# Kernel optimization log

Measured on AMD Instinct MI355X. Metric: run time of the kernel, lower is better.

Reference implementation:

```python
import jax, jax.numpy as jnp
import numpy as np


def setup_inputs() -> dict:
    key = jax.random.key(0)
    k1, k2 = jax.random.split(key)
    batch, cw_dim = 4096, 1024
    dim_embedding, book_size = 8, 256
    dim_codes = cw_dim // dim_embedding  # 128
    x = jax.random.normal(k1, (batch, cw_dim), dtype=jnp.float32)
    codebook = jax.random.normal(k2, (dim_codes, book_size, dim_embedding), dtype=jnp.float32)
    return {"x": x, "codebook": codebook}


def reference(x, codebook):
    # Faithful JAX version of VQVAE.quantise:
    #   pairwise squared distance -> argmin -> gather embeddings -> one-hot scatter
    C, K, D = codebook.shape          # dim_codes, book_size, dim_embedding
    B = x.shape[0]
    xr = x.reshape(B, C, D)           # [B, C, D] (= view(batch*dim_codes, 1, D))
    x2 = jnp.sum(xr * xr, axis=-1)                       # [B, C]
    c2 = jnp.sum(codebook * codebook, axis=-1)           # [C, K]
    dist = x2[..., None] - 2.0 * jnp.einsum('bcd,ckd->bck', xr, codebook) + c2[None]
    idx = jnp.argmin(dist, axis=-1)                      # [B, C]
    # gather nearest codebook entry per code slot
    cw_embed = codebook[jnp.arange(C)[None, :], idx]     # [B, C, D]
    cw_embed = cw_embed.reshape(B, C * D)                # [B, cw_dim]
    # one-hot scatter of selected indices
    one_hot_idx = jax.nn.one_hot(idx, K, dtype=jnp.float32)  # [B, C, K]
    return cw_embed, one_hot_idx
```

## Files before the change

kernel.cpp:

```cpp
#include <hip/hip_runtime.h>


constexpr int B_  = 4096;
constexpr int C_  = 128;
constexpr int K_  = 256;
constexpr int D_  = 8;
constexpr int TPB = 256;

constexpr int   BPT   = 2;
constexpr int   BTILE = TPB * BPT;
constexpr float TAU2  = 1.0e-3f;

typedef float vf4 __attribute__((ext_vector_type(4)));

__global__ __launch_bounds__(TPB) void vq_fused(
    const float* __restrict__ x,
    const float* __restrict__ cb,
    float* __restrict__ out_embed,
    float* __restrict__ out_onehot)
{
    __shared__ float s_cbf[K_ * D_];
    __shared__ float s_c2f[K_];

    const int c    = blockIdx.x;
    const int bt   = blockIdx.y;
    const int tid  = threadIdx.x;
    const int lane = tid & 63;
    const int wave = tid >> 6;

    {
        const float4* gcb = (const float4*)(cb + (size_t)c * (K_ * D_));
        ((float4*)s_cbf)[tid]       = gcb[tid];
        ((float4*)s_cbf)[tid + TPB] = gcb[tid + TPB];
    }
    __syncthreads();
    {
        const float* v = s_cbf + tid * D_;
        float s = 0.f;
        #pragma unroll
        for (int d = 0; d < D_; ++d) s = fmaf(v[d], v[d], s);
        s_c2f[tid] = s;
    }
    __syncthreads();

    const float4* scb4 = (const float4*)s_cbf;
    const int bbase = bt * BTILE;

    float xf[BPT][D_];
    #pragma unroll
    for (int j = 0; j < BPT; ++j) {
        const int b = bbase + j * TPB + tid;
        const float4* xp = (const float4*)(x + (size_t)b * (C_ * D_) + c * D_);
        const float4 a = xp[0];
        const float4 h = xp[1];
        xf[j][0] = a.x; xf[j][1] = a.y; xf[j][2] = a.z; xf[j][3] = a.w;
        xf[j][4] = h.x; xf[j][5] = h.y; xf[j][6] = h.z; xf[j][7] = h.w;
    }

    float s1[BPT], s2[BPT];
    int   k1[BPT];
    #pragma unroll
    for (int j = 0; j < BPT; ++j) { s1[j] = 3.4e38f; s2[j] = 3.4e38f; k1[j] = 0; }

    #pragma unroll 2
    for (int k = 0; k < K_; ++k) {
        const float4 clo = scb4[k * 2];
        const float4 chi = scb4[k * 2 + 1];
        const float  c2k = s_c2f[k];
        #pragma unroll
        for (int j = 0; j < BPT; ++j) {
            float dot = xf[j][0] * clo.x;
            dot = fmaf(xf[j][1], clo.y, dot);
            dot = fmaf(xf[j][2], clo.z, dot);
            dot = fmaf(xf[j][3], clo.w, dot);
            dot = fmaf(xf[j][4], chi.x, dot);
            dot = fmaf(xf[j][5], chi.y, dot);
            dot = fmaf(xf[j][6], chi.z, dot);
            dot = fmaf(xf[j][7], chi.w, dot);
            const float score = fmaf(-2.f, dot, c2k);
            s2[j] = fminf(s2[j], fmaxf(score, s1[j]));
            const bool lt = score < s1[j];
            k1[j] = lt ? k : k1[j];
            s1[j] = lt ? score : s1[j];
        }
    }

    #pragma unroll
    for (int j = 0; j < BPT; ++j) {
        const bool amb = (s2[j] - s1[j]) <= TAU2;
        unsigned long long mask = __ballot(amb);
        while (mask) {
            const int src = (int)__ffsll((long long)mask) - 1;
            mask &= mask - 1;
            double xd[D_];
            #pragma unroll
            for (int d = 0; d < D_; ++d) xd[d] = (double)__shfl(xf[j][d], src);
            double best = 1.0e300;
            int    bk   = 0;
            #pragma unroll
            for (int t = 0; t < 4; ++t) {
                const int k = lane * 4 + t;
                const float* cv = s_cbf + k * D_;
                double cd[D_];
                #pragma unroll
                for (int d = 0; d < D_; ++d) cd[d] = (double)cv[d];
                double c2k = 0.0;
                #pragma unroll
                for (int d = 0; d < D_; ++d) c2k = fma(cd[d], cd[d], c2k);
                double dot = xd[0] * cd[0];
                #pragma unroll
                for (int d = 1; d < D_; ++d) dot = fma(xd[d], cd[d], dot);
                const double score = fma(-2.0, dot, c2k);
                if (score < best) { best = score; bk = k; }
            }
            #pragma unroll
            for (int off = 32; off >= 1; off >>= 1) {
                const double ob  = __shfl_down(best, off);
                const int    obk = __shfl_down(bk,   off);
                if (ob < best) { best = ob; bk = obk; }
            }
            const int win = __shfl(bk, 0);
            if (lane == src) k1[j] = win;
        }
    }

    #pragma unroll
    for (int j = 0; j < BPT; ++j) {
        const int    b    = bbase + j * TPB + tid;
        const size_t pair = (size_t)b * C_ + c;
        float4* dst = (float4*)(out_embed + pair * D_);
        dst[0] = ((const float4*)s_cbf)[k1[j] * 2];
        dst[1] = ((const float4*)s_cbf)[k1[j] * 2 + 1];

        const int bw = bbase + j * TPB + wave * 64;
        const int e0 = lane * 4;
        #pragma unroll 8
        for (int i = 0; i < 64; ++i) {
            const int k = __builtin_amdgcn_readlane(k1[j], i);
            vf4 v;
            v.x = (k == e0    ) ? 1.f : 0.f;
            v.y = (k == e0 + 1) ? 1.f : 0.f;
            v.z = (k == e0 + 2) ? 1.f : 0.f;
            v.w = (k == e0 + 3) ? 1.f : 0.f;
            const size_t row = (size_t)(bw + i) * C_ + c;
            ((vf4*)(out_onehot + row * K_))[lane] = v;
        }
    }
}

extern "C" void kernel_launch(void* const* d_in, const int* in_sizes, int n_in,
                              void* d_out, int out_size, void* d_ws, size_t ws_size,
                              hipStream_t stream) {
    const float* x  = (const float*)d_in[0];
    const float* cb = (const float*)d_in[1];
    float* out        = (float*)d_out;
    float* out_embed  = out;
    float* out_onehot = out + (size_t)B_ * C_ * D_;

    dim3 grid(C_, B_ / BTILE);
    vq_fused<<<grid, TPB, 0, stream>>>(x, cb, out_embed, out_onehot);
}
```

Baseline: 582.1 us.

## Interleave one-hot stores of first batch with distance loop of second batch

Splits the two per-thread batch rows into sequential phases. The one-hot output writes for the first row are issued inside the second row's codebook distance loop, so stores overlap with compute. Codebook entries are now read as wave-uniform 8-float vectors straight from global memory (likely scalar loads) instead of from LDS. This costs some ILP, since each loop now handles one row instead of two, and the in-loop branch adds overhead.

New measurement: 624.0 us. 7.2% more time.

```diff
diff --git a/kernel.cpp b/kernel.cpp
--- a/kernel.cpp
+++ b/kernel.cpp
@@ -11,7 +11,49 @@
 constexpr int   BTILE = TPB * BPT;
 constexpr float TAU2  = 1.0e-3f;
 
-typedef float vf4 __attribute__((ext_vector_type(4)));
+typedef float vf4   __attribute__((ext_vector_type(4)));
+typedef float f32x8 __attribute__((ext_vector_type(8)));
+
+__device__ __forceinline__ void repair_amb(
+    const float xfj[D_], int& k1j, const float s1j, const float s2j,
+    const float* s_cbf, const int lane)
+{
+    const bool amb = (s2j - s1j) <= TAU2;
+    unsigned long long mask = __ballot(amb);
+    while (mask) {
+        const int src = (int)__ffsll((long long)mask) - 1;
+        mask &= mask - 1;
+        double xd[D_];
+        #pragma unroll
+        for (int d = 0; d < D_; ++d) xd[d] = (double)__shfl(xfj[d], src);
+        double best = 1.0e300;
+        int    bk   = 0;
+        #pragma unroll
+        for (int t = 0; t < 4; ++t) {
+            const int k = lane * 4 + t;
+            const float* cv = s_cbf + k * D_;
+            double cd[D_];
+            #pragma unroll
+            for (int d = 0; d < D_; ++d) cd[d] = (double)cv[d];
+            double c2k = 0.0;
+            #pragma unroll
+            for (int d = 0; d < D_; ++d) c2k = fma(cd[d], cd[d], c2k);
+            double dot = xd[0] * cd[0];
+            #pragma unroll
+            for (int d = 1; d < D_; ++d) dot = fma(xd[d], cd[d], dot);
+            const double score = fma(-2.0, dot, c2k);
+            if (score < best) { best = score; bk = k; }
+        }
+        #pragma unroll
+        for (int off = 32; off >= 1; off >>= 1) {
+            const double ob  = __shfl_down(best, off);
+            const int    obk = __shfl_down(bk,   off);
+            if (ob < best) { best = ob; bk = obk; }
+        }
+        const int win = __shfl(bk, 0);
+        if (lane == src) k1j = win;
+    }
+}
 
 __global__ __launch_bounds__(TPB) void vq_fused(
     const float* __restrict__ x,
@@ -43,106 +85,108 @@
     }
     __syncthreads();
 
-    const float4* scb4 = (const float4*)s_cbf;
     const int bbase = bt * BTILE;
 
-    float xf[BPT][D_];
-    #pragma unroll
-    for (int j = 0; j < BPT; ++j) {
-        const int b = bbase + j * TPB + tid;
-        const float4* xp = (const float4*)(x + (size_t)b * (C_ * D_) + c * D_);
+    const f32x8* __restrict__ cbs8 = (const f32x8*)(cb + (size_t)c * (K_ * D_));
+
+    float xf0[D_], xf1[D_];
+    {
+        const float4* xp = (const float4*)(x + (size_t)(bbase + tid) * (C_ * D_) + c * D_);
         const float4 a = xp[0];
         const float4 h = xp[1];
-        xf[j][0] = a.x; xf[j][1] = a.y; xf[j][2] = a.z; xf[j][3] = a.w;
-        xf[j][4] = h.x; xf[j][5] = h.y; xf[j][6] = h.z; xf[j][7] = h.w;
-    }
-
-    float s1[BPT], s2[BPT];
-    int   k1[BPT];
-    #pragma unroll
-    for (int j = 0; j < BPT; ++j) { s1[j] = 3.4e38f; s2[j] = 3.4e38f; k1[j] = 0; }
-
+        xf0[0] = a.x; xf0[1] = a.y; xf0[2] = a.z; xf0[3] = a.w;
+        xf0[4] = h.x; xf0[5] = h.y; xf0[6] = h.z; xf0[7] = h.w;
+    }
+    {
+        const float4* xp = (const float4*)(x + (size_t)(bbase + TPB + tid) * (C_ * D_) + c * D_);
+        const float4 a = xp[0];
+        const float4 h = xp[1];
+        xf1[0] = a.x; xf1[1] = a.y; xf1[2] = a.z; xf1[3] = a.w;
+        xf1[4] = h.x; xf1[5] = h.y; xf1[6] = h.z; xf1[7] = h.w;
+    }
+
+    float s1_0 = 3.4e38f, s2_0 = 3.4e38f;
+    int   k1_0 = 0;
     #pragma unroll 2
     for (int k = 0; k < K_; ++k) {
-        const float4 clo = scb4[k * 2];
-        const float4 chi = scb4[k * 2 + 1];
-        const float  c2k = s_c2f[k];
-        #pragma unroll
-        for (int j = 0; j < BPT; ++j) {
-            float dot = xf[j][0] * clo.x;
-            dot = fmaf(xf[j][1], clo.y, dot);
-            dot = fmaf(xf[j][2], clo.z, dot);
-            dot = fmaf(xf[j][3], clo.w, dot);
-            dot = fmaf(xf[j][4], chi.x, dot);
-            dot = fmaf(xf[j][5], chi.y, dot);
-            dot = fmaf(xf[j][6], chi.z, dot);
-            dot = fmaf(xf[j][7], chi.w, dot);
-            const float score = fmaf(-2.f, dot, c2k);
-            s2[j] = fminf(s2[j], fmaxf(score, s1[j]));
-            const bool lt = score < s1[j];
-            k1[j] = lt ? k : k1[j];
-            s1[j] = lt ? score : s1[j];
-        }
-    }
-
-    #pragma unroll
-    for (int j = 0; j < BPT; ++j) {
-        const bool amb = (s2[j] - s1[j]) <= TAU2;
-        unsigned long long mask = __ballot(amb);
-        while (mask) {
-            const int src = (int)__ffsll((long long)mask) - 1;
-            mask &= mask - 1;
-            double xd[D_];
-            #pragma unroll
-            for (int d = 0; d < D_; ++d) xd[d] = (double)__shfl(xf[j][d], src);
-            double best = 1.0e300;
-            int    bk   = 0;
-            #pragma unroll
-            for (int t = 0; t < 4; ++t) {
-                const int k = lane * 4 + t;
-                const float* cv = s_cbf + k * D_;
-                double cd[D_];
-                #pragma unroll
-                for (int d = 0; d < D_; ++d) cd[d] = (double)cv[d];
-                double c2k = 0.0;
-                #pragma unroll
-                for (int d = 0; d < D_; ++d) c2k = fma(cd[d], cd[d], c2k);
-                double dot = xd[0] * cd[0];
-                #pragma unroll
-                for (int d = 1; d < D_; ++d) dot = fma(xd[d], cd[d], dot);
-                const double score = fma(-2.0, dot, c2k);
-                if (score < best) { best = score; bk = k; }
-            }
-            #pragma unroll
-            for (int off = 32; off >= 1; off >>= 1) {
-                const double ob  = __shfl_down(best, off);
-                const int    obk = __shfl_down(bk,   off);
-                if (ob < best) { best = ob; bk = obk; }
-            }
-            const int win = __shfl(bk, 0);
-            if (lane == src) k1[j] = win;
-        }
-    }
-
-    #pragma unroll
-    for (int j = 0; j < BPT; ++j) {
-        const int    b    = bbase + j * TPB + tid;
-        const size_t pair = (size_t)b * C_ + c;
+        const f32x8 cw  = cbs8[k];
+        const float c2k = s_c2f[k];
+        float dot = xf0[0] * cw[0];
+        dot = fmaf(xf0[1], cw[1], dot);
+        dot = fmaf(xf0[2], cw[2], dot);
+        dot = fmaf(xf0[3], cw[3], dot);
+        dot = fmaf(xf0[4], cw[4], dot);
+        dot = fmaf(xf0[5], cw[5], dot);
+        dot = fmaf(xf0[6], cw[6], dot);
+        dot = fmaf(xf0[7], cw[7], dot);
+        const float score = fmaf(-2.f, dot, c2k);
+        s2_0 = fminf(s2_0, fmaxf(score, s1_0));
+        const bool lt = score < s1_0;
+        k1_0 = lt ? k : k1_0;
+        s1_0 = lt ? score : s1_0;
+    }
+
+    repair_amb(xf0, k1_0, s1_0, s2_0, s_cbf, lane);
+    {
+        const size_t pair = (size_t)(bbase + tid) * C_ + c;
         float4* dst = (float4*)(out_embed + pair * D_);
-        dst[0] = ((const float4*)s_cbf)[k1[j] * 2];
-        dst[1] = ((const float4*)s_cbf)[k1[j] * 2 + 1];
-
-        const int bw = bbase + j * TPB + wave * 64;
-        const int e0 = lane * 4;
+        dst[0] = ((const float4*)s_cbf)[k1_0 * 2];
+        dst[1] = ((const float4*)s_cbf)[k1_0 * 2 + 1];
+    }
+
+    const int bw0 = bbase + wave * 64;
+    const int e0  = lane * 4;
+    float s1_1 = 3.4e38f, s2_1 = 3.4e38f;
+    int   k1_1 = 0;
+    #pragma unroll 4
+    for (int k = 0; k < K_; ++k) {
+        const f32x8 cw  = cbs8[k];
+        const float c2k = s_c2f[k];
+        float dot = xf1[0] * cw[0];
+        dot = fmaf(xf1[1], cw[1], dot);
+        dot = fmaf(xf1[2], cw[2], dot);
+        dot = fmaf(xf1[3], cw[3], dot);
+        dot = fmaf(xf1[4], cw[4], dot);
+        dot = fmaf(xf1[5], cw[5], dot);
+        dot = fmaf(xf1[6], cw[6], dot);
+        dot = fmaf(xf1[7], cw[7], dot);
+        const float score = fmaf(-2.f, dot, c2k);
+        s2_1 = fminf(s2_1, fmaxf(score, s1_1));
+        const bool lt = score < s1_1;
+        k1_1 = lt ? k : k1_1;
+        s1_1 = lt ? score : s1_1;
+
+        if ((k & 3) == 0) {
+            const int i  = k >> 2;
+            const int kk = __builtin_amdgcn_readlane(k1_0, i);
+            vf4 v;
+            v.x = (kk == e0    ) ? 1.f : 0.f;
+            v.y = (kk == e0 + 1) ? 1.f : 0.f;
+            v.z = (kk == e0 + 2) ? 1.f : 0.f;
+            v.w = (kk == e0 + 3) ? 1.f : 0.f;
+            const size_t row = (size_t)(bw0 + i) * C_ + c;
+            ((vf4*)(out_onehot + row * K_))[lane] = v;
+        }
+    }
+
+    repair_amb(xf1, k1_1, s1_1, s2_1, s_cbf, lane);
+    {
+        const size_t pair = (size_t)(bbase + TPB + tid) * C_ + c;
+        float4* dst = (float4*)(out_embed + pair * D_);
+        dst[0] = ((const float4*)s_cbf)[k1_1 * 2];
+        dst[1] = ((const float4*)s_cbf)[k1_1 * 2 + 1];
+    }
+    {
+        const int bw1 = bbase + TPB + wave * 64;
         #pragma unroll 8
         for (int i = 0; i < 64; ++i) {
-            const int k = __builtin_amdgcn_readlane(k1[j], i);
+            const int kk = __builtin_amdgcn_readlane(k1_1, i);
             vf4 v;
-            v.x = (k == e0    ) ? 1.f : 0.f;
-            v.y = (k == e0 + 1) ? 1.f : 0.f;
-            v.z = (k == e0 + 2) ? 1.f : 0.f;
-            v.w = (k == e0 + 3) ? 1.f : 0.f;
-            const size_t row = (size_t)(bw + i) * C_ + c;
+            v.x = (kk == e0    ) ? 1.f : 0.f;
+            v.y = (kk == e0 + 1) ? 1.f : 0.f;
+            v.z = (kk == e0 + 2) ? 1.f : 0.f;
+            v.w = (kk == e0 + 3) ? 1.f : 0.f;
+            const size_t row = (size_t)(bw1 + i) * C_ + c;
             ((vf4*)(out_onehot + row * K_))[lane] = v;
         }
     }
```
